# Kernel tuning notes

Hardware: AMD Instinct MI355X
Metric: run time of the kernel (lower is better)

Reference implementation:

```python
import jax, jax.numpy as jnp
import numpy as np
from jax import lax

jax.config.update("jax_enable_x64", True)

B = 32768          # batch size
NCS = 96           # number of charging stations
NB = 124           # num_buses
S_BASE = 1000.0
MAX_CS = 22.17
MIN_CS = -22.17
MAX_EV_CH = 22.0
MAX_EV_DIS = -22.0
EV_CAP = 70.0
EV_MIN_CAP = 15.0
ITERS = 100
TOL = 1e-06
DT = 15.0 / 60.0   # timescale (hours)


def setup_inputs() -> dict:
    ks = jax.random.split(jax.random.key(0), 12)
    action = jax.random.uniform(ks[0], (B, NCS), dtype=jnp.float32, minval=-1.0, maxval=1.0)
    prices = jax.random.uniform(ks[1], (B, 1), dtype=jnp.float32, minval=0.05, maxval=0.5)
    active = jax.random.uniform(ks[2], (B, NB - 1), dtype=jnp.float32, minval=0.0, maxval=50.0)
    reactive = jax.random.uniform(ks[3], (B, NB - 1), dtype=jnp.float32, minval=0.0, maxval=20.0)
    cap = jax.random.uniform(ks[4], (B, NCS), dtype=jnp.float32, minval=0.0, maxval=EV_CAP)
    cap = cap * (jax.random.uniform(ks[5], (B, NCS)) > 0.2).astype(jnp.float32)
    tleft = jax.random.randint(ks[6], (B, NCS), 1, 10).astype(jnp.float32)
    bus = jax.random.randint(ks[7], (B, NCS), 0, NB - 1).astype(jnp.float32)
    ev = jnp.stack([cap, tleft, bus], axis=-1).reshape(B, 3 * NCS)  # interleaved triples
    state = jnp.concatenate(
        [jnp.zeros((B, 3), jnp.float32), prices, active, reactive, ev], axis=1
    )  # (B, 4 + 2*(NB-1) + 3*NCS) == (B, 538)
    K_re = (0.005 * jax.random.normal(ks[8], (NB - 1, NB - 1))).astype(jnp.float32)
    K_im = (0.005 * jax.random.normal(ks[9], (NB - 1, NB - 1))).astype(jnp.float32)
    L_re = jnp.ones((NB - 1,), jnp.float32)
    L_im = jnp.zeros((NB - 1,), jnp.float32)
    return {"action": action, "state": state, "K_re": K_re, "K_im": K_im, "L_re": L_re, "L_im": L_im}


def _forward(action, state, K_re, K_im, L_re, L_im):
    b, ncs = action.shape
    nb1 = NB - 1
    es = 4 + 2 * nb1  # start of EV state block
    prices = state[:, 3:4]                                    # (B,1), broadcast over stations
    cap = state[:, es:es + 3 * ncs:3]                         # current capacity
    tleft = state[:, es + 1:es + 1 + 3 * ncs:3]               # time left
    bus = state[:, es + 2:es + 2 + 3 * ncs:3].astype(jnp.int32)  # connected bus index
    conn = (cap > 0).astype(action.dtype)
    max_ch = jnp.minimum(MAX_EV_CH, conn * (EV_CAP - cap) / DT)
    max_dis = jnp.maximum(MAX_EV_DIS, conn * (EV_MIN_CAP - cap) / DT)
    pos = jnp.where(action >= 0, 1.0, 0.0).astype(action.dtype)
    power = action * MAX_CS * pos - action * MIN_CS * (1.0 - pos)
    power = jnp.maximum(jnp.minimum(power, max_ch), max_dis)
    costs = (prices * power * DT).sum(axis=1)
    new_cap = jnp.ceil((cap + power * DT) * 100.0) / 100.0
    dep = (tleft == 1).astype(action.dtype)
    user_sat = (-10.0 * dep * (new_cap - EV_CAP) ** 2).sum(axis=1)
    # scatter-add EV power per bus (duplicate indices accumulate, like torch scatter_add)
    ev_bus = jnp.zeros((b, nb1), power.dtype).at[jnp.arange(b)[:, None], bus].add(power)
    ap = state[:, 4:4 + nb1]
    rp = state[:, 4 + nb1:4 + 2 * nb1]
    S = ((ap + ev_bus) / S_BASE + 1j * (rp / S_BASE)).astype(jnp.complex128)  # (B, NB-1)
    K = (K_re + 1j * K_im).astype(jnp.complex128)
    W = (L_re + 1j * L_im).astype(jnp.complex128)
    v_init = jnp.ones((b, nb1), jnp.complex128)

    def run(v0):
        # Z-bus fixed point: v_k = K @ conj(S / v0)^T + W   (batched as bi)
        vk = jnp.einsum('ij,bj->bi', K, jnp.conj(S / v0)) + W
        tol = jnp.max(jnp.abs(jnp.abs(vk) - jnp.abs(v0)))
        return vk, tol

    def body(carry, _):
        v0, done = carry
        def step(v):
            vk, tol = run(v)
            return vk, tol < TOL
        def skip(v):
            return v, jnp.array(True)
        v_next, conv = lax.cond(done, skip, step, v0)
        return (v_next, done | conv), None

    (v_fin, _), _ = lax.scan(body, (v_init, jnp.array(False)), None, length=ITERS)
    vmag = jnp.abs(v_fin)
    voltage_loss = jnp.minimum(0.0, 0.05 - jnp.abs(1.0 - vmag)).sum(axis=1)
    loss = 1000.0 * voltage_loss + costs + user_sat
    return loss.astype(jnp.float32)


def reference(action, state, K_re, K_im, L_re, L_im):
    return _forward(action, state, K_re, K_im, L_re, L_im)
```

## Files before the change

### kernel.cpp

```cpp
#include <hip/hip_runtime.h>

#define NB1   123
#define NCSd  96
#define SW    538
#define TPB   256
#define BT    16
#define STPB  128


__global__ __launch_bounds__(256) void k_norm(const float* __restrict__ Kre,
                                              const float* __restrict__ Kim,
                                              const float* __restrict__ Lre,
                                              const float* __restrict__ Lim,
                                              float* __restrict__ ws) {
    const int tid = threadIdx.x;
    const int w = tid >> 6, l = tid & 63;
    const int wid = blockIdx.x * 4 + w;
    const int j1 = wid, j2 = wid + 64;
    const bool has2 = j2 < NB1;

    const float* kr1 = Kre + j1 * NB1; const float* ki1 = Kim + j1 * NB1;
    float a0 = kr1[l], b0 = ki1[l];
    float a1 = 0.f, b1 = 0.f;
    if (l < NB1 - 64) { a1 = kr1[l + 64]; b1 = ki1[l + 64]; }
    float c0 = 0.f, d0 = 0.f, c1 = 0.f, d1 = 0.f;
    if (has2) {
        const float* kr2 = Kre + j2 * NB1; const float* ki2 = Kim + j2 * NB1;
        c0 = kr2[l]; d0 = ki2[l];
        if (l < NB1 - 64) { c1 = kr2[l + 64]; d1 = ki2[l + 64]; }
    }
    float s1 = fmaf(a0, a0, b0 * b0) + fmaf(a1, a1, b1 * b1);
    float s2 = fmaf(c0, c0, d0 * d0) + fmaf(c1, c1, d1 * d1);
    #pragma unroll
    for (int off = 32; off; off >>= 1) {
        s1 += __shfl_xor(s1, off);
        s2 += __shfl_xor(s2, off);
    }
    float m2 = has2 ? fmaxf(s1, s2) : s1;
    if (l == 0) atomicMax((unsigned*)ws, __float_as_uint(m2));

    if (wid == 0) {
        float dr = Lre[l] - 1.f, di = Lim[l];
        float d2 = fmaf(dr, dr, di * di);
        if (l + 64 < NB1) {
            float dr2 = Lre[l + 64] - 1.f, di2 = Lim[l + 64];
            d2 = fmaxf(d2, fmaf(dr2, dr2, di2 * di2));
        }
        #pragma unroll
        for (int off = 32; off; off >>= 1) d2 = fmaxf(d2, __shfl_xor(d2, off));
        if (l == 0) atomicMax(((unsigned*)ws) + 1, __float_as_uint(d2));
    }
}

__global__ __launch_bounds__(TPB) void k_fast(const float* __restrict__ action,
                                              const float* __restrict__ state,
                                              float* __restrict__ ws,
                                              float* __restrict__ out) {
    __shared__ __align__(16) float st[4][1088];
    __shared__ __align__(16) float sa[4][192];
    __shared__ float ev[4][2][128];

    const int tid = threadIdx.x;
    const int w = tid >> 6, l = tid & 63;
    const long g = (long)blockIdx.x * 4 + w;

    const float4* G4 = (const float4*)(state + g * (2 * SW));
    const float4* A4 = (const float4*)(action + g * (2 * NCSd));
    float4 v0 = G4[l];
    float4 v1 = G4[l + 64];
    float4 v2 = G4[l + 128];
    float4 v3 = G4[l + 192];
    float4 v4 = make_float4(0.f, 0.f, 0.f, 0.f);
    const bool t4 = l < 269 - 256;
    if (t4) v4 = G4[l + 256];
    float4 av = make_float4(0.f, 0.f, 0.f, 0.f);
    const bool ta = l < 48;
    if (ta) av = A4[l];

    ev[w][0][l] = 0.f; if (l < 64) ev[w][0][l + 64] = 0.f;
    ev[w][1][l] = 0.f; ev[w][1][l + 64] = 0.f;

    float4* st4 = (float4*)st[w];
    st4[l] = v0; st4[l + 64] = v1; st4[l + 128] = v2; st4[l + 192] = v3;
    if (t4) st4[l + 256] = v4;
    float4* sa4 = (float4*)sa[w];
    if (ta) sa4[l] = av;
    asm volatile("s_waitcnt lgkmcnt(0)" ::: "memory");

    const int e = l >> 5, li = l & 31;
    const long b = 2 * g + e;
    const float* srow = st[w] + e * SW;
    const float* actp = sa[w] + e * NCSd;
    float* evp = ev[w][e];
    const float pr = srow[3];

    float cost = 0.f, usat = 0.f;
    #pragma unroll
    for (int s = 0; s < 3; ++s) {
        int i = li + 32 * s;
        float cap = srow[250 + 3 * i];
        float tl  = srow[251 + 3 * i];
        int   bus = (int)srow[252 + 3 * i];
        float a   = actp[i];
        float conn = cap > 0.f ? 1.f : 0.f;
        float mch = fminf(22.0f,  conn * (70.0f - cap) * 4.0f);
        float mds = fmaxf(-22.0f, conn * (15.0f - cap) * 4.0f);
        float p = fmaxf(fminf(22.17f * a, mch), mds);
        cost = fmaf(pr * p, 0.25f, cost);
        float nc = ceilf((cap + p * 0.25f) * 100.0f) * 0.01f;
        if (tl == 1.0f) { float d = nc - 70.0f; usat = fmaf(-10.0f * d, d, usat); }
        atomicAdd(&evp[bus], p);
    }
    asm volatile("s_waitcnt lgkmcnt(0)" ::: "memory");

    float s2 = 0.f;
    #pragma unroll
    for (int s = 0; s < 4; ++s) {
        int k = li + 32 * s;
        if (k < NB1) {
            float apv = srow[4 + k] + evp[k];
            float rpv = srow[127 + k];
            s2 = fmaf(apv, apv, fmaf(rpv, rpv, s2));
        }
    }
    #pragma unroll
    for (int off = 16; off; off >>= 1) {
        s2   += __shfl_xor(s2, off);
        cost += __shfl_xor(cost, off);
        usat += __shfl_xor(usat, off);
    }

    float q  = sqrtf(s2) * 0.001f;
    float R  = sqrtf(ws[0]);
    float dW = sqrtf(ws[1]);
    float x  = R * q * 1.001f + 1e-7f;
    float om = 1.0f - dW;
    float disc = om * om - 4.0f * x;
    bool safe = false;
    if (disc > 0.f) {
        float m = 0.5f * (om + sqrtf(disc));
        safe = (dW + x / m) < 0.0495f;
    }

    if (li == 0) out[b] = cost + usat;

    bool flagged = (li == 0) && !safe;
    unsigned long long mask = __ballot(flagged);
    if (mask) {
        int nf = __popcll(mask);
        int lead = __ffsll((long long)mask) - 1;
        unsigned base_ = 0;
        if (l == lead) base_ = atomicAdd(((unsigned*)ws) + 2, (unsigned)nf);
        base_ = __shfl(base_, lead);
        if (flagged) {
            int rank = __popcll(mask & ((1ull << l) - 1ull));
            ((unsigned*)ws)[3 + base_ + rank] = (unsigned)b;
        }
    }
}

__global__ __launch_bounds__(STPB) void k_solve(const float* __restrict__ action,
                                                const float* __restrict__ state,
                                                const float* __restrict__ Kre,
                                                const float* __restrict__ Kim,
                                                const float* __restrict__ Lre,
                                                const float* __restrict__ Lim,
                                                const float* __restrict__ ws,
                                                float* __restrict__ out) {
    __shared__ float ev[BT][STPB];
    __shared__ __align__(16) float2 cmat[STPB][BT + 2];
    __shared__ float vls[STPB][BT + 1];
    __shared__ float red[2];
    __shared__ unsigned idxs[BT];
    const unsigned count = ((const unsigned*)ws)[2];
    const int tid = threadIdx.x;
    const int j = tid;
    const bool jok = j < NB1;
    const float Wre = jok ? Lre[j] : 1.f;
    const float Wim = jok ? Lim[j] : 0.f;

    for (unsigned base = (unsigned)blockIdx.x * BT; base < count; base += (unsigned)gridDim.x * BT) {
        unsigned nv = count - base; if (nv > BT) nv = BT;
        if (tid < BT) {
            unsigned t = (unsigned)tid < nv ? (unsigned)tid : nv - 1;
            idxs[tid] = ((const unsigned*)ws)[3 + base + t];
        }
        for (int x = tid; x < BT * STPB; x += STPB) ((float*)ev)[x] = 0.f;
        __syncthreads();

        for (int task = tid; task < BT * NCSd; task += STPB) {
            int e = task / NCSd, i = task - e * NCSd;
            long b = (long)idxs[e];
            const float* srow = state + b * SW;
            float cap = srow[250 + 3 * i];
            int   bus = (int)srow[252 + 3 * i];
            float a   = action[b * NCSd + i];
            float conn = cap > 0.f ? 1.f : 0.f;
            float mch = fminf(22.0f,  conn * (70.0f - cap) * 4.0f);
            float mds = fmaxf(-22.0f, conn * (15.0f - cap) * 4.0f);
            float p = fmaxf(fminf(22.17f * a, mch), mds);
            atomicAdd(&ev[e][bus], p);
        }
        __syncthreads();

        float Sre[BT], Sim[BT], vr[BT], vi[BT];
        #pragma unroll
        for (int e = 0; e < BT; ++e) {
            long b = (long)idxs[e];
            float ap = jok ? state[b * SW + 4 + j]   : 0.f;
            float rp = jok ? state[b * SW + 127 + j] : 0.f;
            Sre[e] = (ap + ev[e][j]) * 0.001f;
            Sim[e] = rp * 0.001f;
            vr[e] = 1.f; vi[e] = 0.f;
        }
        for (int it = 0; it < 100; ++it) {
            #pragma unroll
            for (int e = 0; e < BT; ++e) {
                float d = vr[e] * vr[e] + vi[e] * vi[e];
                float inv = 1.0f / d;
                cmat[j][e] = make_float2((Sre[e] * vr[e] + Sim[e] * vi[e]) * inv,
                                         (Sre[e] * vi[e] - Sim[e] * vr[e]) * inv);
            }
            __syncthreads();
            float ar[BT], ai[BT];
            #pragma unroll
            for (int e = 0; e < BT; ++e) { ar[e] = Wre; ai[e] = Wim; }
            for (int k = 0; k < NB1; ++k) {
                float kr = jok ? Kre[j * NB1 + k] : 0.f;
                float ki = jok ? Kim[j * NB1 + k] : 0.f;
                const float4* crow = (const float4*)(&cmat[k][0]);
                #pragma unroll
                for (int eh = 0; eh < BT / 2; ++eh) {
                    float4 c2 = crow[eh];
                    ar[2*eh]   = fmaf(kr, c2.x, fmaf(-ki, c2.y, ar[2*eh]));
                    ai[2*eh]   = fmaf(kr, c2.y, fmaf( ki, c2.x, ai[2*eh]));
                    ar[2*eh+1] = fmaf(kr, c2.z, fmaf(-ki, c2.w, ar[2*eh+1]));
                    ai[2*eh+1] = fmaf(kr, c2.w, fmaf( ki, c2.z, ai[2*eh+1]));
                }
            }
            float md = 0.f;
            #pragma unroll
            for (int e = 0; e < BT; ++e) {
                float vmn = sqrtf(ar[e]*ar[e] + ai[e]*ai[e]);
                float vmo = sqrtf(vr[e]*vr[e] + vi[e]*vi[e]);
                md = fmaxf(md, fabsf(vmn - vmo));
                vr[e] = ar[e]; vi[e] = ai[e];
            }
            #pragma unroll
            for (int off = 32; off; off >>= 1) md = fmaxf(md, __shfl_xor(md, off));
            if ((tid & 63) == 0) red[tid >> 6] = md;
            __syncthreads();
            if (fmaxf(red[0], red[1]) < 1e-6f) break;
        }
        #pragma unroll
        for (int e = 0; e < BT; ++e) {
            float vm = sqrtf(vr[e]*vr[e] + vi[e]*vi[e]);
            vls[j][e] = jok ? fminf(0.f, 0.05f - fabsf(1.0f - vm)) : 0.f;
        }
        __syncthreads();
        if (tid < (int)nv) {
            float s = 0.f;
            for (int k = 0; k < NB1; ++k) s += vls[k][tid];
            long b = (long)idxs[tid];
            out[b] += 1000.0f * s;
        }
        __syncthreads();
    }
}

__global__ __launch_bounds__(STPB) void k_main(
    const float* __restrict__ action, const float* __restrict__ state,
    const float* __restrict__ Kre, const float* __restrict__ Kim,
    const float* __restrict__ Lre, const float* __restrict__ Lim,
    float* __restrict__ out)
{
    __shared__ float ev[BT][STPB];
    __shared__ float costs_s[BT];
    __shared__ float usat_s[BT];
    __shared__ __align__(16) float2 cmat[STPB][BT + 2];
    __shared__ float vls[STPB][BT + 1];
    __shared__ float red[2];
    const int tid = threadIdx.x;
    const int e0  = blockIdx.x * BT;
    for (int x = tid; x < BT * STPB; x += STPB) ((float*)ev)[x] = 0.f;
    if (tid < BT) { costs_s[tid] = 0.f; usat_s[tid] = 0.f; }
    __syncthreads();
    for (int task = tid; task < BT * NCSd; task += STPB) {
        int e = task / NCSd, i = task - e * NCSd;
        long b = (long)(e0 + e);
        const float* srow = state + b * SW;
        float cap = srow[250 + 3 * i], tleft = srow[251 + 3 * i];
        int bus = (int)srow[252 + 3 * i];
        float a = action[b * NCSd + i];
        float conn = cap > 0.f ? 1.f : 0.f;
        float mch = fminf(22.0f, conn * (70.0f - cap) * 4.0f);
        float mds = fmaxf(-22.0f, conn * (15.0f - cap) * 4.0f);
        float power = fmaxf(fminf(22.17f * a, mch), mds);
        atomicAdd(&costs_s[e], srow[3] * power * 0.25f);
        float nc = ceilf((cap + power * 0.25f) * 100.0f) * 0.01f;
        if (tleft == 1.0f) { float d = nc - 70.0f; atomicAdd(&usat_s[e], -10.0f * d * d); }
        atomicAdd(&ev[e][bus], power);
    }
    __syncthreads();
    const int j = tid;
    const bool jok = j < NB1;
    float Wre = jok ? Lre[j] : 1.0f, Wim = jok ? Lim[j] : 0.0f;
    float Sre[BT], Sim[BT], vr[BT], vi[BT];
    #pragma unroll
    for (int e = 0; e < BT; ++e) {
        long b = (long)(e0 + e);
        float ap = jok ? state[b * SW + 4 + j] : 0.f;
        float rp = jok ? state[b * SW + 127 + j] : 0.f;
        Sre[e] = (ap + ev[e][j]) * 0.001f; Sim[e] = rp * 0.001f;
        vr[e] = 1.f; vi[e] = 0.f;
    }
    for (int it = 0; it < 100; ++it) {
        #pragma unroll
        for (int e = 0; e < BT; ++e) {
            float d = vr[e]*vr[e] + vi[e]*vi[e];
            float inv = 1.0f / d;
            cmat[j][e] = make_float2((Sre[e]*vr[e] + Sim[e]*vi[e]) * inv,
                                     (Sre[e]*vi[e] - Sim[e]*vr[e]) * inv);
        }
        __syncthreads();
        float ar[BT], ai[BT];
        #pragma unroll
        for (int e = 0; e < BT; ++e) { ar[e] = Wre; ai[e] = Wim; }
        for (int k = 0; k < NB1; ++k) {
            float kr = jok ? Kre[j*NB1+k] : 0.f;
            float ki = jok ? Kim[j*NB1+k] : 0.f;
            const float4* crow = (const float4*)(&cmat[k][0]);
            #pragma unroll
            for (int eh = 0; eh < BT / 2; ++eh) {
                float4 c2 = crow[eh];
                ar[2*eh]   = fmaf(kr, c2.x, fmaf(-ki, c2.y, ar[2*eh]));
                ai[2*eh]   = fmaf(kr, c2.y, fmaf( ki, c2.x, ai[2*eh]));
                ar[2*eh+1] = fmaf(kr, c2.z, fmaf(-ki, c2.w, ar[2*eh+1]));
                ai[2*eh+1] = fmaf(kr, c2.w, fmaf( ki, c2.z, ai[2*eh+1]));
            }
        }
        float md = 0.f;
        #pragma unroll
        for (int e = 0; e < BT; ++e) {
            float vmn = sqrtf(ar[e]*ar[e] + ai[e]*ai[e]);
            float vmo = sqrtf(vr[e]*vr[e] + vi[e]*vi[e]);
            md = fmaxf(md, fabsf(vmn - vmo));
            vr[e] = ar[e]; vi[e] = ai[e];
        }
        #pragma unroll
        for (int off = 32; off > 0; off >>= 1) md = fmaxf(md, __shfl_xor(md, off));
        if ((tid & 63) == 0) red[tid >> 6] = md;
        __syncthreads();
        if (fmaxf(red[0], red[1]) < 1e-6f) break;
    }
    #pragma unroll
    for (int e = 0; e < BT; ++e) {
        float vm = sqrtf(vr[e]*vr[e] + vi[e]*vi[e]);
        vls[j][e] = jok ? fminf(0.f, 0.05f - fabsf(1.0f - vm)) : 0.f;
    }
    __syncthreads();
    if (tid < BT) {
        float s = 0.f;
        for (int k = 0; k < NB1; ++k) s += vls[k][tid];
        out[e0 + tid] = 1000.0f * s + costs_s[tid] + usat_s[tid];
    }
}

extern "C" void kernel_launch(void* const* d_in, const int* in_sizes, int n_in,
                              void* d_out, int out_size, void* d_ws, size_t ws_size,
                              hipStream_t stream) {
    const float* action = (const float*)d_in[0];
    const float* state  = (const float*)d_in[1];
    const float* Kre    = (const float*)d_in[2];
    const float* Kim    = (const float*)d_in[3];
    const float* Lre    = (const float*)d_in[4];
    const float* Lim    = (const float*)d_in[5];
    float* out = (float*)d_out;
    const int B = out_size;

    const size_t wsNeed = (size_t)(3 + B) * sizeof(unsigned);
    if (ws_size >= wsNeed) {
        float* ws = (float*)d_ws;
        hipMemsetAsync(d_ws, 0, 12, stream);
        hipLaunchKernelGGL(k_norm, dim3(16), dim3(256), 0, stream, Kre, Kim, Lre, Lim, ws);
        hipLaunchKernelGGL(k_fast, dim3(B / 8), dim3(TPB), 0, stream,
                           action, state, ws, out);
        hipLaunchKernelGGL(k_solve, dim3(64), dim3(STPB), 0, stream,
                           action, state, Kre, Kim, Lre, Lim, ws, out);
    } else {
        hipLaunchKernelGGL(k_main, dim3((B + BT - 1) / BT), dim3(STPB), 0, stream,
                           action, state, Kre, Kim, Lre, Lim, out);
    }
}
```

Baseline: 40.04 us.

## Fold norm prep into one block, precompute safety threshold, drop memset

The norm kernel becomes a single 512-thread block that reduces the K row norms and the W deviation in shared memory. It precomputes a squared-load threshold so the per-row safety test in k_fast is one comparison, and it resets the flag counter itself, which removes the separate memset launch. k_fast now reads action directly from global memory instead of staging it in shared memory, and the solve grid shrinks from 64 to 8 blocks. The risks are small float differences in the threshold inversion and less parallelism if many rows get flagged.

```diff
diff --git a/kernel.cpp b/kernel.cpp
--- a/kernel.cpp
+++ b/kernel.cpp
@@ -8,47 +8,60 @@
 #define STPB  128
 
 
-__global__ __launch_bounds__(256) void k_norm(const float* __restrict__ Kre,
+__global__ __launch_bounds__(512) void k_prep(const float* __restrict__ Kre,
                                               const float* __restrict__ Kim,
                                               const float* __restrict__ Lre,
                                               const float* __restrict__ Lim,
                                               float* __restrict__ ws) {
+    __shared__ float wred[16];
     const int tid = threadIdx.x;
     const int w = tid >> 6, l = tid & 63;
-    const int wid = blockIdx.x * 4 + w;
-    const int j1 = wid, j2 = wid + 64;
-    const bool has2 = j2 < NB1;
-
-    const float* kr1 = Kre + j1 * NB1; const float* ki1 = Kim + j1 * NB1;
-    float a0 = kr1[l], b0 = ki1[l];
-    float a1 = 0.f, b1 = 0.f;
-    if (l < NB1 - 64) { a1 = kr1[l + 64]; b1 = ki1[l + 64]; }
-    float c0 = 0.f, d0 = 0.f, c1 = 0.f, d1 = 0.f;
-    if (has2) {
-        const float* kr2 = Kre + j2 * NB1; const float* ki2 = Kim + j2 * NB1;
-        c0 = kr2[l]; d0 = ki2[l];
-        if (l < NB1 - 64) { c1 = kr2[l + 64]; d1 = ki2[l + 64]; }
-    }
-    float s1 = fmaf(a0, a0, b0 * b0) + fmaf(a1, a1, b1 * b1);
-    float s2 = fmaf(c0, c0, d0 * d0) + fmaf(c1, c1, d1 * d1);
-    #pragma unroll
-    for (int off = 32; off; off >>= 1) {
-        s1 += __shfl_xor(s1, off);
-        s2 += __shfl_xor(s2, off);
-    }
-    float m2 = has2 ? fmaxf(s1, s2) : s1;
-    if (l == 0) atomicMax((unsigned*)ws, __float_as_uint(m2));
-
-    if (wid == 0) {
+    float rmax2 = 0.f;
+    for (int j = w; j < NB1; j += 8) {
+        const float* kr = Kre + j * NB1;
+        const float* ki = Kim + j * NB1;
+        float a = kr[l], bb = ki[l];
+        float s = fmaf(a, a, bb * bb);
+        if (l + 64 < NB1) {
+            float a2 = kr[l + 64], b2 = ki[l + 64];
+            s = fmaf(a2, a2, fmaf(b2, b2, s));
+        }
+        #pragma unroll
+        for (int off = 32; off; off >>= 1) s += __shfl_xor(s, off);
+        rmax2 = fmaxf(rmax2, s);
+    }
+    float dw2 = 0.f;
+    if (w == 0) {
         float dr = Lre[l] - 1.f, di = Lim[l];
-        float d2 = fmaf(dr, dr, di * di);
+        dw2 = fmaf(dr, dr, di * di);
         if (l + 64 < NB1) {
             float dr2 = Lre[l + 64] - 1.f, di2 = Lim[l + 64];
-            d2 = fmaxf(d2, fmaf(dr2, dr2, di2 * di2));
-        }
-        #pragma unroll
-        for (int off = 32; off; off >>= 1) d2 = fmaxf(d2, __shfl_xor(d2, off));
-        if (l == 0) atomicMax(((unsigned*)ws) + 1, __float_as_uint(d2));
+            dw2 = fmaxf(dw2, fmaf(dr2, dr2, di2 * di2));
+        }
+        #pragma unroll
+        for (int off = 32; off; off >>= 1) dw2 = fmaxf(dw2, __shfl_xor(dw2, off));
+    }
+    if (l == 0) { wred[w] = rmax2; wred[8 + w] = dw2; }
+    __syncthreads();
+    if (tid == 0) {
+        float r2 = wred[0];
+        #pragma unroll
+        for (int i = 1; i < 8; ++i) r2 = fmaxf(r2, wred[i]);
+        float R  = sqrtf(r2);
+        float dW = sqrtf(wred[8]);
+        float t = 0.0495f - dW;
+        float q2max = -1.0f;
+        if (t > 0.f && t < 1.0f - dW) {
+            float xm = t * (1.0f - dW - t);
+            xm = (xm - 1e-7f) / 1.001f;
+            if (xm > 0.f && R > 0.f) {
+                float qmax = xm / R;
+                float sm = qmax * 1000.0f;
+                q2max = sm * sm;
+            }
+        }
+        ws[0] = q2max;
+        ((unsigned*)ws)[1] = 0u;
     }
 }
 
@@ -57,15 +70,13 @@
                                               float* __restrict__ ws,
                                               float* __restrict__ out) {
     __shared__ __align__(16) float st[4][1088];
-    __shared__ __align__(16) float sa[4][192];
-    __shared__ float ev[4][2][128];
+    __shared__ float ev[4][256];
 
     const int tid = threadIdx.x;
     const int w = tid >> 6, l = tid & 63;
     const long g = (long)blockIdx.x * 4 + w;
 
     const float4* G4 = (const float4*)(state + g * (2 * SW));
-    const float4* A4 = (const float4*)(action + g * (2 * NCSd));
     float4 v0 = G4[l];
     float4 v1 = G4[l + 64];
     float4 v2 = G4[l + 128];
@@ -73,25 +84,20 @@
     float4 v4 = make_float4(0.f, 0.f, 0.f, 0.f);
     const bool t4 = l < 269 - 256;
     if (t4) v4 = G4[l + 256];
-    float4 av = make_float4(0.f, 0.f, 0.f, 0.f);
-    const bool ta = l < 48;
-    if (ta) av = A4[l];
-
-    ev[w][0][l] = 0.f; if (l < 64) ev[w][0][l + 64] = 0.f;
-    ev[w][1][l] = 0.f; ev[w][1][l + 64] = 0.f;
+
+    ev[w][l] = 0.f; ev[w][l + 64] = 0.f;
+    ev[w][l + 128] = 0.f; ev[w][l + 192] = 0.f;
 
     float4* st4 = (float4*)st[w];
     st4[l] = v0; st4[l + 64] = v1; st4[l + 128] = v2; st4[l + 192] = v3;
     if (t4) st4[l + 256] = v4;
-    float4* sa4 = (float4*)sa[w];
-    if (ta) sa4[l] = av;
     asm volatile("s_waitcnt lgkmcnt(0)" ::: "memory");
 
     const int e = l >> 5, li = l & 31;
     const long b = 2 * g + e;
     const float* srow = st[w] + e * SW;
-    const float* actp = sa[w] + e * NCSd;
-    float* evp = ev[w][e];
+    const float* actp = action + b * NCSd;
+    float* evp = ev[w] + e * 128;
     const float pr = srow[3];
 
     float cost = 0.f, usat = 0.f;
@@ -130,18 +136,7 @@
         usat += __shfl_xor(usat, off);
     }
 
-    float q  = sqrtf(s2) * 0.001f;
-    float R  = sqrtf(ws[0]);
-    float dW = sqrtf(ws[1]);
-    float x  = R * q * 1.001f + 1e-7f;
-    float om = 1.0f - dW;
-    float disc = om * om - 4.0f * x;
-    bool safe = false;
-    if (disc > 0.f) {
-        float m = 0.5f * (om + sqrtf(disc));
-        safe = (dW + x / m) < 0.0495f;
-    }
-
+    bool safe = s2 <= ws[0];
     if (li == 0) out[b] = cost + usat;
 
     bool flagged = (li == 0) && !safe;
@@ -150,11 +145,11 @@
         int nf = __popcll(mask);
         int lead = __ffsll((long long)mask) - 1;
         unsigned base_ = 0;
-        if (l == lead) base_ = atomicAdd(((unsigned*)ws) + 2, (unsigned)nf);
+        if (l == lead) base_ = atomicAdd(((unsigned*)ws) + 1, (unsigned)nf);
         base_ = __shfl(base_, lead);
         if (flagged) {
             int rank = __popcll(mask & ((1ull << l) - 1ull));
-            ((unsigned*)ws)[3 + base_ + rank] = (unsigned)b;
+            ((unsigned*)ws)[2 + base_ + rank] = (unsigned)b;
         }
     }
 }
@@ -172,7 +167,7 @@
     __shared__ float vls[STPB][BT + 1];
     __shared__ float red[2];
     __shared__ unsigned idxs[BT];
-    const unsigned count = ((const unsigned*)ws)[2];
+    const unsigned count = ((const unsigned*)ws)[1];
     const int tid = threadIdx.x;
     const int j = tid;
     const bool jok = j < NB1;
@@ -183,7 +178,7 @@
         unsigned nv = count - base; if (nv > BT) nv = BT;
         if (tid < BT) {
             unsigned t = (unsigned)tid < nv ? (unsigned)tid : nv - 1;
-            idxs[tid] = ((const unsigned*)ws)[3 + base + t];
+            idxs[tid] = ((const unsigned*)ws)[2 + base + t];
         }
         for (int x = tid; x < BT * STPB; x += STPB) ((float*)ev)[x] = 0.f;
         __syncthreads();
@@ -378,14 +373,13 @@
     float* out = (float*)d_out;
     const int B = out_size;
 
-    const size_t wsNeed = (size_t)(3 + B) * sizeof(unsigned);
+    const size_t wsNeed = (size_t)(2 + B) * sizeof(unsigned);
     if (ws_size >= wsNeed) {
         float* ws = (float*)d_ws;
-        hipMemsetAsync(d_ws, 0, 12, stream);
-        hipLaunchKernelGGL(k_norm, dim3(16), dim3(256), 0, stream, Kre, Kim, Lre, Lim, ws);
+        hipLaunchKernelGGL(k_prep, dim3(1), dim3(512), 0, stream, Kre, Kim, Lre, Lim, ws);
         hipLaunchKernelGGL(k_fast, dim3(B / 8), dim3(TPB), 0, stream,
                            action, state, ws, out);
-        hipLaunchKernelGGL(k_solve, dim3(64), dim3(STPB), 0, stream,
+        hipLaunchKernelGGL(k_solve, dim3(8), dim3(STPB), 0, stream,
                            action, state, Kre, Kim, Lre, Lim, ws, out);
     } else {
         hipLaunchKernelGGL(k_main, dim3((B + BT - 1) / BT), dim3(STPB), 0, stream,
```

Measured after the change: 46.49 us. 1.16x slower.

## Drop memset via per-block norm partials, read action directly, precompute safety threshold

Applied to the files above, without the earlier changes.

Removes the hipMemsetAsync launch. k_norm now writes each block's max row norm to its own workspace slot and resets the counter itself, and k_fast reduces those 16 partials with shuffles. k_fast no longer stages the action row in shared memory and reads it straight from global memory. The per-row quadratic safety test is replaced by a comparison of s2 against a threshold derived once per wave, and the k_solve grid shrinks from 64 to 16 blocks. The counter reset depends on k_norm finishing before k_fast on the same stream, and the new threshold test may flag slightly different rows at the boundary than the old one.

```diff
diff --git a/kernel.cpp b/kernel.cpp
--- a/kernel.cpp
+++ b/kernel.cpp
@@ -13,6 +13,7 @@
                                               const float* __restrict__ Lre,
                                               const float* __restrict__ Lim,
                                               float* __restrict__ ws) {
+    __shared__ float part[4];
     const int tid = threadIdx.x;
     const int w = tid >> 6, l = tid & 63;
     const int wid = blockIdx.x * 4 + w;
@@ -37,9 +38,12 @@
         s2 += __shfl_xor(s2, off);
     }
     float m2 = has2 ? fmaxf(s1, s2) : s1;
-    if (l == 0) atomicMax((unsigned*)ws, __float_as_uint(m2));
-
-    if (wid == 0) {
+    if (l == 0) part[w] = m2;
+    __syncthreads();
+    if (tid == 0)
+        ws[2 + blockIdx.x] = fmaxf(fmaxf(part[0], part[1]), fmaxf(part[2], part[3]));
+
+    if (blockIdx.x == 0 && w == 0) {
         float dr = Lre[l] - 1.f, di = Lim[l];
         float d2 = fmaf(dr, dr, di * di);
         if (l + 64 < NB1) {
@@ -48,7 +52,7 @@
         }
         #pragma unroll
         for (int off = 32; off; off >>= 1) d2 = fmaxf(d2, __shfl_xor(d2, off));
-        if (l == 0) atomicMax(((unsigned*)ws) + 1, __float_as_uint(d2));
+        if (l == 0) { ws[1] = d2; ((unsigned*)ws)[0] = 0u; }
     }
 }
 
@@ -57,15 +61,13 @@
                                               float* __restrict__ ws,
                                               float* __restrict__ out) {
     __shared__ __align__(16) float st[4][1088];
-    __shared__ __align__(16) float sa[4][192];
-    __shared__ float ev[4][2][128];
+    __shared__ float ev[4][256];
 
     const int tid = threadIdx.x;
     const int w = tid >> 6, l = tid & 63;
     const long g = (long)blockIdx.x * 4 + w;
 
     const float4* G4 = (const float4*)(state + g * (2 * SW));
-    const float4* A4 = (const float4*)(action + g * (2 * NCSd));
     float4 v0 = G4[l];
     float4 v1 = G4[l + 64];
     float4 v2 = G4[l + 128];
@@ -73,25 +75,23 @@
     float4 v4 = make_float4(0.f, 0.f, 0.f, 0.f);
     const bool t4 = l < 269 - 256;
     if (t4) v4 = G4[l + 256];
-    float4 av = make_float4(0.f, 0.f, 0.f, 0.f);
-    const bool ta = l < 48;
-    if (ta) av = A4[l];
-
-    ev[w][0][l] = 0.f; if (l < 64) ev[w][0][l + 64] = 0.f;
-    ev[w][1][l] = 0.f; ev[w][1][l + 64] = 0.f;
+
+    float r2p = (l < 16) ? ws[2 + l] : 0.f;
+    float dw2 = ws[1];
+
+    ev[w][l] = 0.f; ev[w][l + 64] = 0.f;
+    ev[w][l + 128] = 0.f; ev[w][l + 192] = 0.f;
 
     float4* st4 = (float4*)st[w];
     st4[l] = v0; st4[l + 64] = v1; st4[l + 128] = v2; st4[l + 192] = v3;
     if (t4) st4[l + 256] = v4;
-    float4* sa4 = (float4*)sa[w];
-    if (ta) sa4[l] = av;
     asm volatile("s_waitcnt lgkmcnt(0)" ::: "memory");
 
     const int e = l >> 5, li = l & 31;
     const long b = 2 * g + e;
     const float* srow = st[w] + e * SW;
-    const float* actp = sa[w] + e * NCSd;
-    float* evp = ev[w][e];
+    const float* actp = action + b * NCSd;
+    float* evp = ev[w] + e * 128;
     const float pr = srow[3];
 
     float cost = 0.f, usat = 0.f;
@@ -130,17 +130,20 @@
         usat += __shfl_xor(usat, off);
     }
 
-    float q  = sqrtf(s2) * 0.001f;
-    float R  = sqrtf(ws[0]);
-    float dW = sqrtf(ws[1]);
-    float x  = R * q * 1.001f + 1e-7f;
-    float om = 1.0f - dW;
-    float disc = om * om - 4.0f * x;
-    bool safe = false;
-    if (disc > 0.f) {
-        float m = 0.5f * (om + sqrtf(disc));
-        safe = (dW + x / m) < 0.0495f;
-    }
+    #pragma unroll
+    for (int off = 8; off; off >>= 1) r2p = fmaxf(r2p, __shfl_xor(r2p, off));
+    float R  = sqrtf(__shfl(r2p, 0));
+    float dW = sqrtf(dw2);
+    float t = 0.0495f - dW;
+    float q2max = -1.0f;
+    if (t > 0.f && t < 1.0f - dW) {
+        float xm = (t * (1.0f - dW - t) - 1e-7f) / 1.001f;
+        if (xm > 0.f && R > 0.f) {
+            float sm = xm / R * 1000.0f;
+            q2max = sm * sm;
+        }
+    }
+    bool safe = s2 <= q2max;
 
     if (li == 0) out[b] = cost + usat;
 
@@ -150,11 +153,11 @@
         int nf = __popcll(mask);
         int lead = __ffsll((long long)mask) - 1;
         unsigned base_ = 0;
-        if (l == lead) base_ = atomicAdd(((unsigned*)ws) + 2, (unsigned)nf);
+        if (l == lead) base_ = atomicAdd((unsigned*)ws, (unsigned)nf);
         base_ = __shfl(base_, lead);
         if (flagged) {
             int rank = __popcll(mask & ((1ull << l) - 1ull));
-            ((unsigned*)ws)[3 + base_ + rank] = (unsigned)b;
+            ((unsigned*)ws)[18 + base_ + rank] = (unsigned)b;
         }
     }
 }
@@ -172,7 +175,7 @@
     __shared__ float vls[STPB][BT + 1];
     __shared__ float red[2];
     __shared__ unsigned idxs[BT];
-    const unsigned count = ((const unsigned*)ws)[2];
+    const unsigned count = ((const unsigned*)ws)[0];
     const int tid = threadIdx.x;
     const int j = tid;
     const bool jok = j < NB1;
@@ -183,7 +186,7 @@
         unsigned nv = count - base; if (nv > BT) nv = BT;
         if (tid < BT) {
             unsigned t = (unsigned)tid < nv ? (unsigned)tid : nv - 1;
-            idxs[tid] = ((const unsigned*)ws)[3 + base + t];
+            idxs[tid] = ((const unsigned*)ws)[18 + base + t];
         }
         for (int x = tid; x < BT * STPB; x += STPB) ((float*)ev)[x] = 0.f;
         __syncthreads();
@@ -378,14 +381,13 @@
     float* out = (float*)d_out;
     const int B = out_size;
 
-    const size_t wsNeed = (size_t)(3 + B) * sizeof(unsigned);
+    const size_t wsNeed = (size_t)(18 + B) * sizeof(unsigned);
     if (ws_size >= wsNeed) {
         float* ws = (float*)d_ws;
-        hipMemsetAsync(d_ws, 0, 12, stream);
         hipLaunchKernelGGL(k_norm, dim3(16), dim3(256), 0, stream, Kre, Kim, Lre, Lim, ws);
         hipLaunchKernelGGL(k_fast, dim3(B / 8), dim3(TPB), 0, stream,
                            action, state, ws, out);
-        hipLaunchKernelGGL(k_solve, dim3(64), dim3(STPB), 0, stream,
+        hipLaunchKernelGGL(k_solve, dim3(16), dim3(STPB), 0, stream,
                            action, state, Kre, Kim, Lre, Lim, ws, out);
     } else {
         hipLaunchKernelGGL(k_main, dim3((B + BT - 1) / BT), dim3(STPB), 0, stream,
```

New measurement: 37.71 us. 1.06x faster.
